# Optimization experiments

Hardware: AMD Instinct MI355X
Metric: run time of the kernel (lower is better)

The kernel has to match this reference:

```python
import jax, jax.numpy as jnp
import numpy as np

B, S, H, E, T, L = 128, 1024, 512, 512, 64, 128


def setup_inputs() -> dict:
    key = jax.random.key(0)
    ks = jax.random.split(key, 20)
    s = 0.02
    inp = {
        "sent_lengths": jax.random.randint(ks[0], (B,), 1, S, dtype=jnp.int32),
        "output_length": T,
        "decoder_input": jax.random.normal(ks[1], (B, E), jnp.float32),
        "h0": jax.random.normal(ks[2], (B, H), jnp.float32),
        "c0": jax.random.normal(ks[3], (B, H), jnp.float32),
        "context": jax.random.normal(ks[4], (B, S, H), jnp.float32),
        "cur_labels": jax.random.randint(ks[5], (B, T), 0, L, dtype=jnp.int32),
        "cur_max_nsymbs": jax.random.randint(ks[6], (B,), 0, 10, dtype=jnp.int32),
        # parameters
        "label_emb": jax.random.normal(ks[7], (L, E), jnp.float32) * s,
        "W_ih": jax.random.normal(ks[8], (4 * H, E), jnp.float32) * s,
        "b_ih": jnp.zeros((4 * H,), jnp.float32),
        "W_hh": jax.random.normal(ks[9], (4 * H, H), jnp.float32) * s,
        "b_hh": jnp.zeros((4 * H,), jnp.float32),
        "W_ho": jax.random.normal(ks[10], (H, 2 * H), jnp.float32) * s,
        "b_ho": jnp.zeros((H,), jnp.float32),
        "W_attn_in": jax.random.normal(ks[11], (H, H), jnp.float32) * s,
        "b_attn_in": jnp.zeros((H,), jnp.float32),
        "W_attn_ctx": jax.random.normal(ks[12], (H, H), jnp.float32) * s,
        "b_attn_ctx": jnp.zeros((H,), jnp.float32),
        "V": jax.random.uniform(ks[13], (H,), jnp.float32, -1.0, 1.0),
        "W_out": jax.random.normal(ks[14], (L, 2 * H + E), jnp.float32) * s,
        "b_out": jnp.zeros((L,), jnp.float32),
    }
    # padding_idx row of the label embedding is zero (torch nn.Embedding semantics)
    inp["label_emb"] = inp["label_emb"].at[0].set(0.0)
    return inp


def _decode(output_length, decoder_input, h0, c0, context, cur_labels,
            label_emb, W_ih, b_ih, W_hh, b_hh, W_ho, b_ho,
            W_attn_in, b_attn_in, W_attn_ctx, b_attn_ctx, V, W_out, b_out):
    # Precompute the 1x1-conv context projection once (identical math to per-step conv).
    ctx = jnp.einsum("bsh,gh->bsg", context, W_attn_ctx) + b_attn_ctx  # [B,S,H]

    # Teacher-forced input sequence: x_0 = decoder_input, x_i = emb(labels[:, i-1]).
    emb = label_emb[cur_labels]                     # [B,T,E]
    xs = jnp.concatenate(
        [decoder_input[None], jnp.swapaxes(emb, 0, 1)[: output_length - 1]], axis=0
    )                                               # [T,B,E]

    def step(carry, x):
        h, c = carry
        gates = x @ W_ih.T + b_ih + h @ W_hh.T + b_hh          # [B,4H]
        i_g, f_g, g_g, o_g = jnp.split(gates, 4, axis=1)
        c_t = jax.nn.sigmoid(f_g) * c + jax.nn.sigmoid(i_g) * jnp.tanh(g_g)
        h_lstm = jax.nn.sigmoid(o_g) * jnp.tanh(c_t)            # [B,H]
        # pointer attention
        inp = h_lstm @ W_attn_in.T + b_attn_in                  # [B,H]
        att = jnp.einsum("bsh,h->bs", jnp.tanh(inp[:, None, :] + ctx), V)
        alpha = jax.nn.softmax(att, axis=-1)                    # [B,S]
        weighted = jnp.einsum("bs,bsh->bh", alpha, ctx)         # [B,H]
        hidden_t = jnp.tanh(jnp.concatenate([weighted, h_lstm], 1) @ W_ho.T + b_ho)
        out = jnp.concatenate([hidden_t, weighted, x], 1) @ W_out.T + b_out  # [B,L]
        return (hidden_t, c_t), out

    (h_f, c_f), outs = jax.lax.scan(step, (h0, c0), xs)  # outs [T,B,L]
    outputs = jnp.transpose(outs, (1, 0, 2))             # [B,T,L]
    preds = jnp.argmax(outputs, axis=-1)                 # [B,T]
    return outputs, preds, h_f, c_f


def reference(sent_lengths, output_length, decoder_input, h0, c0, context,
              cur_labels, cur_max_nsymbs, label_emb, W_ih, b_ih, W_hh, b_hh,
              W_ho, b_ho, W_attn_in, b_attn_in, W_attn_ctx, b_attn_ctx, V,
              W_out, b_out):
    # cur_batch_len = len(sent_lengths) == B, so hidden slicing is a no-op here.
    # cur_max_nsymbs unused (constrained_decoding=None path).
    return _decode(output_length, decoder_input, h0, c0, context, cur_labels,
                   label_emb, W_ih, b_ih, W_hh, b_hh, W_ho, b_ho,
                   W_attn_in, b_attn_in, W_attn_ctx, b_attn_ctx, V, W_out, b_out)
```

## Files before the change

kernel.cpp:

```cpp
#include <hip/hip_runtime.h>
#include <hip/hip_bf16.h>
#include <math.h>

#define B_ 128
#define S_ 1024
#define H_ 512
#define E_ 512
#define T_ 64
#define L_ 128
#define G4H 2048
#define QS 8

typedef __attribute__((ext_vector_type(8))) short bf16x8;
typedef __attribute__((ext_vector_type(4))) float f32x4;

__device__ inline float sigmoidf_(float x) { return 1.f / (1.f + expf(-x)); }
__device__ inline float fast_tanhf_(float x) {
    float e = __expf(2.f * x);
    return 1.f - 2.f / (e + 1.f);
}
__device__ inline unsigned f2bf1(float f) {
    unsigned u = __float_as_uint(f);
    return (u + 0x7fffu + ((u >> 16) & 1u)) >> 16;
}

#define LDP 40
__global__ __launch_bounds__(256) void gemm_split(
    const float* __restrict__ A, int lda,
    const float* __restrict__ W, int ldw,
    const float* __restrict__ bias,
    const float* __restrict__ Cinit, int ldci,
    float* __restrict__ C, int ldc,
    int K, int act, int perm)
{
    __shared__ unsigned short Ah[128 * LDP];
    __shared__ unsigned short Al[128 * LDP];
    __shared__ unsigned short Bh[128 * LDP];
    __shared__ unsigned short Bl[128 * LDP];
    const int n0 = blockIdx.x * 128;
    const int m0 = blockIdx.y * 128;
    const int t = threadIdx.x;
    const int lane = t & 63, wv = t >> 6;
    const int wr = wv >> 1, wc = wv & 1;
    const int row = t >> 1, koff = (t & 1) * 16;

    f32x4 acc[4][4] = {};

    float av[16], wvv[16];
    {
        const float* ap = A + (size_t)(m0 + row) * lda + koff;
        const float* wp = W + (size_t)(n0 + row) * ldw + koff;
#pragma unroll
        for (int q = 0; q < 4; ++q) {
            *reinterpret_cast<float4*>(&av[q * 4]) = *reinterpret_cast<const float4*>(ap + q * 4);
            *reinterpret_cast<float4*>(&wvv[q * 4]) = *reinterpret_cast<const float4*>(wp + q * 4);
        }
// ... 62 lines not shown
            const float bs = bias ? bias[n] : 0.f;
#pragma unroll
            for (int r = 0; r < 4; ++r) {
                const int m = m0 + wr * 64 + i * 16 + (lane >> 4) * 4 + r;
                float v = acc[i][j][r] + bs;
                if (Cinit) v += Cinit[(size_t)m * ldci + n];
                if (act == 1) v = tanhf(v);
                size_t crow;
                if (perm) { int bb = m & 127, tt = m >> 7; crow = ((size_t)bb * T_ + tt) * ldc; }
                else crow = (size_t)m * ldc;
                C[crow + n] = v;
            }
        }
}

__global__ __launch_bounds__(128) void k_perm(
    const float* __restrict__ W_ih, const float* __restrict__ W_hh,
    const float* __restrict__ b_ih, const float* __restrict__ b_hh,
    float* __restrict__ Wip, float* __restrict__ Whp, float* __restrict__ bp)
{
    int rp = blockIdx.x;
    int h = rp >> 2, g = rp & 3;
    int src = g * 512 + h;
    int t = threadIdx.x;
    const float4* si = reinterpret_cast<const float4*>(W_ih + (size_t)src * 512);
    const float4* sh = reinterpret_cast<const float4*>(W_hh + (size_t)src * 512);
    float4* di = reinterpret_cast<float4*>(Wip + (size_t)rp * 512);
    float4* dh = reinterpret_cast<float4*>(Whp + (size_t)rp * 512);
    di[t] = si[t];
    dh[t] = sh[t];
    if (t == 0) bp[rp] = b_ih[src] + b_hh[src];
}

__global__ __launch_bounds__(256) void k_gateslstm(
    const float* __restrict__ hbuf,
    const float* __restrict__ Whp,
    const float* __restrict__ xproj_t,
    float* __restrict__ cbuf,
    float* __restrict__ hlstm)
{
    __shared__ float As[16][32];
    __shared__ float Ws[16][64];
    const int n0 = blockIdx.x * 64;
    const int m0 = blockIdx.y * 32;
    const int t = threadIdx.x;
    const int tx = t & 15;
    const int ty = t >> 4;
    const int alr = t >> 3, alk = (t & 7) * 2;
    const int wlr = t >> 2, wlk = (t & 3) * 4;

    float acc[2][4] = {};

    float2 pa = *reinterpret_cast<const float2*>(hbuf + (size_t)(m0 + alr) * 512 + alk);
    float4 pv = *reinterpret_cast<const float4*>(Whp + (size_t)(n0 + wlr) * 512 + wlk);

    for (int k0 = 0; k0 < 512; k0 += 16) {
        __syncthreads();
        As[alk + 0][alr] = pa.x; As[alk + 1][alr] = pa.y;
        Ws[wlk + 0][wlr] = pv.x; Ws[wlk + 1][wlr] = pv.y;
        Ws[wlk + 2][wlr] = pv.z; Ws[wlk + 3][wlr] = pv.w;
        __syncthreads();
        if (k0 + 16 < 512) {
            pa = *reinterpret_cast<const float2*>(hbuf + (size_t)(m0 + alr) * 512 + k0 + 16 + alk);
            pv = *reinterpret_cast<const float4*>(Whp + (size_t)(n0 + wlr) * 512 + k0 + 16 + wlk);
        }
#pragma unroll
        for (int kk = 0; kk < 16; ++kk) {
            float a[2], b[4];
            a[0] = As[kk][ty * 2]; a[1] = As[kk][ty * 2 + 1];
#pragma unroll
            for (int j = 0; j < 4; ++j) b[j] = Ws[kk][tx * 4 + j];
#pragma unroll
            for (int i = 0; i < 2; ++i)
#pragma unroll
                for (int j = 0; j < 4; ++j) acc[i][j] = fmaf(a[i], b[j], acc[i][j]);
        }
    }

    const int h = (n0 >> 2) + tx;
#pragma unroll
    for (int i = 0; i < 2; ++i) {
        const int b = m0 + ty * 2 + i;
        float4 xp = *reinterpret_cast<const float4*>(xproj_t + (size_t)b * G4H + n0 + tx * 4);
        float ig = sigmoidf_(acc[i][0] + xp.x);
        float fg = sigmoidf_(acc[i][1] + xp.y);
        float gg = tanhf(acc[i][2] + xp.z);
        float og = sigmoidf_(acc[i][3] + xp.w);
        float c = fg * cbuf[(size_t)b * 512 + h] + ig * gg;
        cbuf[(size_t)b * 512 + h] = c;
        hlstm[(size_t)b * 512 + h] = og * tanhf(c);
    }
}

__global__ __launch_bounds__(256) void gemm_stepk(
    const float* __restrict__ A, int lda,
    const float* __restrict__ W, int ldw,
    float* __restrict__ P, int N, int Kc)
{
    __shared__ float As[16][128];
    __shared__ float Ws[16][64];
    const int n0 = blockIdx.x * 64;
    const int k0 = blockIdx.y * Kc;
    const int t = threadIdx.x;
    const int tx = t & 15;
    const int ty = t >> 4;
    const int ar = t >> 1, akq = (t & 1) * 8;
    const int wr = t >> 2, wkq = (t & 3) * 4;

    float acc[8][4] = {};

    float4 a0 = *reinterpret_cast<const float4*>(A + (size_t)ar * lda + k0 + akq);
    float4 a1 = *reinterpret_cast<const float4*>(A + (size_t)ar * lda + k0 + akq + 4);
    float4 w0 = *reinterpret_cast<const float4*>(W + (size_t)(n0 + wr) * ldw + k0 + wkq);

    for (int kb = 0; kb < Kc; kb += 16) {
        __syncthreads();
        As[akq + 0][ar] = a0.x; As[akq + 1][ar] = a0.y; As[akq + 2][ar] = a0.z; As[akq + 3][ar] = a0.w;
        As[akq + 4][ar] = a1.x; As[akq + 5][ar] = a1.y; As[akq + 6][ar] = a1.z; As[akq + 7][ar] = a1.w;
        Ws[wkq + 0][wr] = w0.x; Ws[wkq + 1][wr] = w0.y; Ws[wkq + 2][wr] = w0.z; Ws[wkq + 3][wr] = w0.w;
        __syncthreads();
        if (kb + 16 < Kc) {
            a0 = *reinterpret_cast<const float4*>(A + (size_t)ar * lda + k0 + kb + 16 + akq);
            a1 = *reinterpret_cast<const float4*>(A + (size_t)ar * lda + k0 + kb + 16 + akq + 4);
            w0 = *reinterpret_cast<const float4*>(W + (size_t)(n0 + wr) * ldw + k0 + kb + 16 + wkq);
        }
#pragma unroll
        for (int kk = 0; kk < 16; ++kk) {
            float a[8], b[4];
#pragma unroll
            for (int i = 0; i < 8; ++i) a[i] = As[kk][ty * 8 + i];
#pragma unroll
            for (int j = 0; j < 4; ++j) b[j] = Ws[kk][tx * 4 + j];
#pragma unroll
            for (int i = 0; i < 8; ++i)
#pragma unroll
                for (int j = 0; j < 4; ++j) acc[i][j] = fmaf(a[i], b[j], acc[i][j]);
        }
    }

#pragma unroll
    for (int i = 0; i < 8; ++i) {
        const int m = ty * 8 + i;
#pragma unroll
        for (int j = 0; j < 4; ++j)
            P[((size_t)blockIdx.y * 128 + m) * N + n0 + tx * 4 + j] = acc[i][j];
    }
}

__global__ __launch_bounds__(256) void k_who(
    const float* __restrict__ pm, const float* __restrict__ pl,
    const float* __restrict__ pw, const float* __restrict__ hlstm,
    const float* __restrict__ W_ho,
    float* __restrict__ P, float* __restrict__ hist_t)
{
    __shared__ float As[16][128];
    __shared__ float Ws[16][64];
    __shared__ float eql[128][QS];
    const int n0 = blockIdx.x * 64;
    const int k0 = blockIdx.y * 128;
    const int t = threadIdx.x;
    const int tx = t & 15;
    const int ty = t >> 4;
    const int ar = t >> 1, akq = (t & 1) * 8;
    const int wr = t >> 2, wkq = (t & 3) * 4;
    const bool merge_side = (k0 < 512);
    const bool writer = (blockIdx.x == 0) && merge_side;

    if (merge_side && t < 128) {
        float mq[QS], eq[QS];
        float M = -INFINITY;
#pragma unroll
        for (int q = 0; q < QS; ++q) { mq[q] = pm[QS * t + q]; M = fmaxf(M, mq[q]); }
        float Lt = 0.f;
#pragma unroll
        for (int q = 0; q < QS; ++q) { eq[q] = __expf(mq[q] - M); Lt += eq[q] * pl[QS * t + q]; }
        float inv = 1.f / Lt;
#pragma unroll
        for (int q = 0; q < QS; ++q) eql[t][q] = eq[q] * inv;
    }
    __syncthreads();

    float acc[8][4] = {};
    float av[8];
    float4 w0;

    auto load_stage = [&](int kb) {
        const int kg = k0 + kb + akq;
        if (merge_side) {
#pragma unroll
            for (int e = 0; e < 8; ++e) av[e] = 0.f;
#pragma unroll
            for (int q = 0; q < QS; ++q) {
                const float* pr = pw + (size_t)(QS * ar + q) * 512 + kg;
                float4 pa = *reinterpret_cast<const float4*>(pr);
                float4 pb = *reinterpret_cast<const float4*>(pr + 4);
                float qw = eql[ar][q];
                av[0] = fmaf(qw, pa.x, av[0]); av[1] = fmaf(qw, pa.y, av[1]);
                av[2] = fmaf(qw, pa.z, av[2]); av[3] = fmaf(qw, pa.w, av[3]);
                av[4] = fmaf(qw, pb.x, av[4]); av[5] = fmaf(qw, pb.y, av[5]);
                av[6] = fmaf(qw, pb.z, av[6]); av[7] = fmaf(qw, pb.w, av[7]);
            }
            if (writer) {
                *reinterpret_cast<float4*>(hist_t + (size_t)ar * 1024 + 512 + kg) = *reinterpret_cast<float4*>(&av[0]);
                *reinterpret_cast<float4*>(hist_t + (size_t)ar * 1024 + 512 + kg + 4) = *reinterpret_cast<float4*>(&av[4]);
            }
        } else {
            *reinterpret_cast<float4*>(&av[0]) = *reinterpret_cast<const float4*>(hlstm + (size_t)ar * 512 + kg - 512);
            *reinterpret_cast<float4*>(&av[4]) = *reinterpret_cast<const float4*>(hlstm + (size_t)ar * 512 + kg - 512 + 4);
        }
        w0 = *reinterpret_cast<const float4*>(W_ho + (size_t)(n0 + wr) * 1024 + k0 + kb + wkq);
    };

    load_stage(0);

    for (int kb = 0; kb < 128; kb += 16) {
        __syncthreads();
        As[akq + 0][ar] = av[0]; As[akq + 1][ar] = av[1]; As[akq + 2][ar] = av[2]; As[akq + 3][ar] = av[3];
        As[akq + 4][ar] = av[4]; As[akq + 5][ar] = av[5]; As[akq + 6][ar] = av[6]; As[akq + 7][ar] = av[7];
        Ws[wkq + 0][wr] = w0.x; Ws[wkq + 1][wr] = w0.y; Ws[wkq + 2][wr] = w0.z; Ws[wkq + 3][wr] = w0.w;
        __syncthreads();
        if (kb + 16 < 128) load_stage(kb + 16);
#pragma unroll
        for (int kk = 0; kk < 16; ++kk) {
            float a[8], b[4];
#pragma unroll
            for (int i = 0; i < 8; ++i) a[i] = As[kk][ty * 8 + i];
#pragma unroll
            for (int j = 0; j < 4; ++j) b[j] = Ws[kk][tx * 4 + j];
#pragma unroll
            for (int i = 0; i < 8; ++i)
#pragma unroll
                for (int j = 0; j < 4; ++j) acc[i][j] = fmaf(a[i], b[j], acc[i][j]);
        }
    }

#pragma unroll
    for (int i = 0; i < 8; ++i) {
        const int m = ty * 8 + i;
#pragma unroll
        for (int j = 0; j < 4; ++j)
            P[((size_t)blockIdx.y * 128 + m) * 512 + n0 + tx * 4 + j] = acc[i][j];
    }
}

__global__ void k_embed(const float* __restrict__ dec_in, const int* __restrict__ labels,
                        const float* __restrict__ emb, float* __restrict__ X)
{
    size_t total = (size_t)T_ * B_ * E_;
    for (size_t i = (size_t)blockIdx.x * blockDim.x + threadIdx.x; i < total;
         i += (size_t)gridDim.x * blockDim.x) {
        int e = (int)(i % E_);
        int b = (int)((i / E_) % B_);
        int t = (int)(i / ((size_t)E_ * B_));
        float v;
        if (t == 0) v = dec_in[b * E_ + e];
        else {
            int lab = labels[b * T_ + (t - 1)];
            v = emb[(size_t)lab * E_ + e];
        }
        X[i] = v;
    }
}

__global__ void k_init(const float* __restrict__ h0, const float* __restrict__ c0,
                       float* __restrict__ hbuf, float* __restrict__ cbuf)
{
    int i = blockIdx.x * blockDim.x + threadIdx.x;
    hbuf[i] = h0[i];
    cbuf[i] = c0[i];
}

__global__ __launch_bounds__(512) void k_attn(const float* __restrict__ ctx,
    const float* __restrict__ Pa, const float* __restrict__ b_ain,
    const float* __restrict__ Vv,
    float* __restrict__ pm, float* __restrict__ pl, float* __restrict__ pw)
{
    int blk = blockIdx.x;
    int b = blk >> 3, q = blk & 7;
    int tid = threadIdx.x, lane = tid & 63, wv = tid >> 6;

    __shared__ float inp_sh[512];
    inp_sh[tid] = Pa[(size_t)b * 512 + tid]
                + Pa[(size_t)(128 + b) * 512 + tid]
                + Pa[(size_t)(256 + b) * 512 + tid]
                + Pa[(size_t)(384 + b) * 512 + tid]
                + b_ain[tid];
    __syncthreads();

    float inpr[8], vr[8];
    {
        const float4* v4 = reinterpret_cast<const float4*>(Vv) + lane * 2;
        *(float4*)&vr[0] = v4[0];   *(float4*)&vr[4] = v4[1];
#pragma unroll
        for (int k = 0; k < 8; ++k) inpr[k] = inp_sh[lane * 8 + k];
    }
    const float* sp = ctx + ((size_t)b * S_ + q * 128 + wv * 16) * H_ + lane * 8;

    float m = -INFINITY, l = 0.f, w[8] = {};
    float4 c0 = *reinterpret_cast<const float4*>(sp);
    float4 c1 = *reinterpret_cast<const float4*>(sp + 4);
    for (int si = 0; si < 16; ++si) {
        float4 u0 = c0, u1 = c1;
        if (si < 15) {
            c0 = *reinterpret_cast<const float4*>(sp + (size_t)(si + 1) * H_);
            c1 = *reinterpret_cast<const float4*>(sp + (size_t)(si + 1) * H_ + 4);
        }
        float c8[8];
        *(float4*)&c8[0] = u0; *(float4*)&c8[4] = u1;
        float t = 0.f;
#pragma unroll
        for (int k = 0; k < 8; ++k) t = fmaf(fast_tanhf_(inpr[k] + c8[k]), vr[k], t);
#pragma unroll
        for (int off = 32; off > 0; off >>= 1) t += __shfl_xor(t, off);
        float mn = fmaxf(m, t);
        float sc = __expf(m - mn);
        float p  = __expf(t - mn);
        l = l * sc + p;
#pragma unroll
        for (int k = 0; k < 8; ++k) w[k] = w[k] * sc + p * c8[k];
        m = mn;
    }

    __shared__ float wl[8 * 512];
    __shared__ float ml[8], ll[8];
#pragma unroll
    for (int k = 0; k < 8; ++k) wl[wv * 512 + lane * 8 + k] = w[k];
    if (lane == 0) { ml[wv] = m; ll[wv] = l; }
    __syncthreads();

    float M = ml[0];
#pragma unroll
    for (int u = 1; u < 8; ++u) M = fmaxf(M, ml[u]);
    float lt = 0.f, wt = 0.f;
#pragma unroll
    for (int u = 0; u < 8; ++u) {
        float e = __expf(ml[u] - M);
        lt += e * ll[u];
        wt += e * wl[u * 512 + tid];
    }
    if (tid == 0) { pm[blk] = M; pl[blk] = lt; }
    pw[(size_t)blk * 512 + tid] = wt;
}

__global__ __launch_bounds__(256) void k_whofin(const float* __restrict__ Po,
    const float* __restrict__ b_ho, float* __restrict__ hbuf, float* __restrict__ hist_t)
{
    int i = blockIdx.x * blockDim.x + threadIdx.x;
    int b = i >> 9, h = i & 511;
    float v = b_ho[h];
#pragma unroll
    for (int ks = 0; ks < 8; ++ks) v += Po[((size_t)ks * 128 + b) * 512 + h];
    v = tanhf(v);
    hbuf[i] = v;
    hist_t[(size_t)b * 1024 + h] = v;
}

__global__ __launch_bounds__(128) void k_argmax(const float* __restrict__ outp,
                                                float* __restrict__ preds)
{
    int row = blockIdx.x;
    int tid = threadIdx.x;
    float v = outp[(size_t)row * L_ + tid];
    int idx = tid;
#pragma unroll
    for (int off = 32; off > 0; off >>= 1) {
        float ov = __shfl_xor(v, off);
        int oi = __shfl_xor(idx, off);
        if (ov > v || (ov == v && oi < idx)) { v = ov; idx = oi; }
    }
    __shared__ float sv[2];
    __shared__ int si[2];
    if ((tid & 63) == 0) { sv[tid >> 6] = v; si[tid >> 6] = idx; }
    __syncthreads();
    if (tid == 0) {
        float v0 = sv[0], v1 = sv[1];
        int i0 = si[0], i1 = si[1];
        int r = (v1 > v0 || (v1 == v0 && i1 < i0)) ? i1 : i0;
        preds[row] = (float)r;
    }
}

__global__ void k_final(const float* __restrict__ hbuf, const float* __restrict__ cbuf,
                        float* __restrict__ hf, float* __restrict__ cf)
{
    int i = blockIdx.x * blockDim.x + threadIdx.x;
    hf[i] = hbuf[i];
    cf[i] = cbuf[i];
}

extern "C" void kernel_launch(void* const* d_in, const int* in_sizes, int n_in,
                              void* d_out, int out_size, void* d_ws, size_t ws_size,
                              hipStream_t stream)
{
    const float* dec_in  = (const float*)d_in[2];
    const float* h0      = (const float*)d_in[3];
    const float* c0      = (const float*)d_in[4];
    const float* context = (const float*)d_in[5];
    const int*   labels  = (const int*)d_in[6];
    const float* emb     = (const float*)d_in[8];
    const float* W_ih    = (const float*)d_in[9];
    const float* b_ih    = (const float*)d_in[10];
    const float* W_hh    = (const float*)d_in[11];
    const float* b_hh    = (const float*)d_in[12];
    const float* W_ho    = (const float*)d_in[13];
    const float* b_ho    = (const float*)d_in[14];
    const float* W_ain   = (const float*)d_in[15];
    const float* b_ain   = (const float*)d_in[16];
    const float* W_actx  = (const float*)d_in[17];
    const float* b_actx  = (const float*)d_in[18];
    const float* Vv      = (const float*)d_in[19];
    const float* W_out   = (const float*)d_in[20];
    const float* b_out   = (const float*)d_in[21];

    float* ws = (float*)d_ws;
    float* X     = ws; ws += (size_t)T_ * B_ * E_;
    float* xproj = ws; ws += (size_t)T_ * B_ * G4H;
    float* xout  = ws; ws += (size_t)T_ * B_ * L_;
    float* ctx   = ws; ws += (size_t)B_ * S_ * H_;
    float* hist  = ws; ws += (size_t)T_ * B_ * 1024;
    float* Wip   = ws; ws += (size_t)G4H * 512;
    float* Whp   = ws; ws += (size_t)G4H * 512;
    float* bp    = ws; ws += G4H;
    float* Pa    = ws; ws += (size_t)4 * B_ * H_;
    float* Po    = ws; ws += (size_t)8 * B_ * H_;
    float* cbuf  = ws; ws += (size_t)B_ * H_;
    float* hbuf  = ws; ws += (size_t)B_ * H_;
    float* hlstm = ws; ws += (size_t)B_ * H_;
    float* pm    = ws; ws += (size_t)B_ * QS;
    float* pl    = ws; ws += (size_t)B_ * QS;
    float* pw    = ws; ws += (size_t)B_ * QS * 512;

    float* out_logits = (float*)d_out;
    float* out_preds  = out_logits + (size_t)B_ * T_ * L_;
    float* out_hf     = out_preds + (size_t)B_ * T_;
    float* out_cf     = out_hf + (size_t)B_ * H_;

    k_embed<<<2048, 256, 0, stream>>>(dec_in, labels, emb, X);
    k_init<<<256, 256, 0, stream>>>(h0, c0, hbuf, cbuf);
    k_perm<<<G4H, 128, 0, stream>>>(W_ih, W_hh, b_ih, b_hh, Wip, Whp, bp);
    gemm_split<<<dim3(16, 64), 256, 0, stream>>>(X, E_, Wip, E_, bp, nullptr, 0,
                                                 xproj, G4H, E_, 0, 0);
    gemm_split<<<dim3(1, 64), 256, 0, stream>>>(X, E_, W_out + 1024, 1536, b_out, nullptr, 0,
                                                xout, L_, E_, 0, 0);
    gemm_split<<<dim3(4, 1024), 256, 0, stream>>>(context, H_, W_actx, H_, b_actx, nullptr, 0,
                                                  ctx, H_, H_, 0, 0);

    for (int t = 0; t < T_; ++t) {
        float* hist_t = hist + (size_t)t * B_ * 1024;
        k_gateslstm<<<dim3(32, 4), 256, 0, stream>>>(hbuf, Whp,
                                                     xproj + (size_t)t * B_ * G4H,
                                                     cbuf, hlstm);
        gemm_stepk<<<dim3(8, 4), 256, 0, stream>>>(hlstm, H_, W_ain, H_, Pa, H_, 128);
        k_attn<<<B_ * QS, 512, 0, stream>>>(ctx, Pa, b_ain, Vv, pm, pl, pw);
        k_who<<<dim3(8, 8), 256, 0, stream>>>(pm, pl, pw, hlstm, W_ho, Po, hist_t);
        k_whofin<<<256, 256, 0, stream>>>(Po, b_ho, hbuf, hist_t);
    }

    gemm_split<<<dim3(1, 64), 256, 0, stream>>>(hist, 1024, W_out, 1536, nullptr,
                                                xout, L_, out_logits, L_, 1024, 0, 1);
    k_argmax<<<B_ * T_, 128, 0, stream>>>(out_logits, out_preds);
    k_final<<<256, 256, 0, stream>>>(hbuf, cbuf, out_hf, out_cf);
}
```

Baseline: 7.470 ms.

## Fuse hidden-state finalization into LSTM gate kernel and split attention projection further

Removes the per-step k_whofin launch. The next step's k_gateslstm now reduces the W_ho split-K partials, applies tanh on the fly while loading its A operand, and has block column 0 write the history row for the previous step. The last step's finalization moves into a single k_fin63 kernel that also writes the final h/c outputs, which replaces k_final. The attention-input projection GEMM is also split into 8 K-slices instead of 4 to launch more blocks, and k_attn sums the 8 partials. In exchange, every gate block redundantly recomputes the 8-way reduction and tanh for its A tiles, which adds global reads and transcendental work inside the recurrent loop.

After: 8.467 ms. +13.4%, slower.

```diff
diff --git a/kernel.cpp b/kernel.cpp
--- a/kernel.cpp
+++ b/kernel.cpp
@@ -152,10 +152,14 @@
 
 __global__ __launch_bounds__(256) void k_gateslstm(
     const float* __restrict__ hbuf,
+    const float* __restrict__ Po,
+    const float* __restrict__ b_ho,
     const float* __restrict__ Whp,
     const float* __restrict__ xproj_t,
     float* __restrict__ cbuf,
-    float* __restrict__ hlstm)
+    float* __restrict__ hlstm,
+    float* __restrict__ hist_prev,
+    int fused)
 {
     __shared__ float As[16][32];
     __shared__ float Ws[16][64];
@@ -169,7 +173,22 @@
 
     float acc[2][4] = {};
 
-    float2 pa = *reinterpret_cast<const float2*>(hbuf + (size_t)(m0 + alr) * 512 + alk);
+    auto load_pa = [&](int k0) -> float2 {
+        const int row = m0 + alr, k = k0 + alk;
+        if (!fused) return *reinterpret_cast<const float2*>(hbuf + (size_t)row * 512 + k);
+        float s0 = b_ho[k], s1 = b_ho[k + 1];
+#pragma unroll
+        for (int ks = 0; ks < 8; ++ks) {
+            float2 p = *reinterpret_cast<const float2*>(Po + ((size_t)ks * 128 + row) * 512 + k);
+            s0 += p.x; s1 += p.y;
+        }
+        float2 r; r.x = tanhf(s0); r.y = tanhf(s1);
+        if (blockIdx.x == 0)
+            *reinterpret_cast<float2*>(hist_prev + (size_t)row * 1024 + k) = r;
+        return r;
+    };
+
+    float2 pa = load_pa(0);
     float4 pv = *reinterpret_cast<const float4*>(Whp + (size_t)(n0 + wlr) * 512 + wlk);
 
     for (int k0 = 0; k0 < 512; k0 += 16) {
@@ -179,7 +198,7 @@
         Ws[wlk + 2][wlr] = pv.z; Ws[wlk + 3][wlr] = pv.w;
         __syncthreads();
         if (k0 + 16 < 512) {
-            pa = *reinterpret_cast<const float2*>(hbuf + (size_t)(m0 + alr) * 512 + k0 + 16 + alk);
+            pa = load_pa(k0 + 16);
             pv = *reinterpret_cast<const float4*>(Whp + (size_t)(n0 + wlr) * 512 + k0 + 16 + wlk);
         }
 #pragma unroll
@@ -398,11 +417,12 @@
     int tid = threadIdx.x, lane = tid & 63, wv = tid >> 6;
 
     __shared__ float inp_sh[512];
-    inp_sh[tid] = Pa[(size_t)b * 512 + tid]
-                + Pa[(size_t)(128 + b) * 512 + tid]
-                + Pa[(size_t)(256 + b) * 512 + tid]
-                + Pa[(size_t)(384 + b) * 512 + tid]
-                + b_ain[tid];
+    {
+        float s = b_ain[tid];
+#pragma unroll
+        for (int ks = 0; ks < 8; ++ks) s += Pa[((size_t)ks * 128 + b) * 512 + tid];
+        inp_sh[tid] = s;
+    }
     __syncthreads();
 
     float inpr[8], vr[8];
@@ -415,6 +435,24 @@
     const float* sp = ctx + ((size_t)b * S_ + q * 128 + wv * 16) * H_ + lane * 8;
 
     float m = -INFINITY, l = 0.f, w[8] = {};
+
+    auto process = [&](float4 u0, float4 u1) {
+        float c8[8];
+        *(float4*)&c8[0] = u0; *(float4*)&c8[4] = u1;
+        float t = 0.f;
+#pragma unroll
+        for (int k = 0; k < 8; ++k) t = fmaf(fast_tanhf_(inpr[k] + c8[k]), vr[k], t);
+#pragma unroll
+        for (int off = 32; off > 0; off >>= 1) t += __shfl_xor(t, off);
+        float mn = fmaxf(m, t);
+        float sc = __expf(m - mn);
+        float p  = __expf(t - mn);
+        l = l * sc + p;
+#pragma unroll
+        for (int k = 0; k < 8; ++k) w[k] = w[k] * sc + p * c8[k];
+        m = mn;
+    };
+
     float4 c0 = *reinterpret_cast<const float4*>(sp);
     float4 c1 = *reinterpret_cast<const float4*>(sp + 4);
     for (int si = 0; si < 16; ++si) {
@@ -423,20 +461,7 @@
             c0 = *reinterpret_cast<const float4*>(sp + (size_t)(si + 1) * H_);
             c1 = *reinterpret_cast<const float4*>(sp + (size_t)(si + 1) * H_ + 4);
         }
-        float c8[8];
-        *(float4*)&c8[0] = u0; *(float4*)&c8[4] = u1;
-        float t = 0.f;
-#pragma unroll
-        for (int k = 0; k < 8; ++k) t = fmaf(fast_tanhf_(inpr[k] + c8[k]), vr[k], t);
-#pragma unroll
-        for (int off = 32; off > 0; off >>= 1) t += __shfl_xor(t, off);
-        float mn = fmaxf(m, t);
-        float sc = __expf(m - mn);
-        float p  = __expf(t - mn);
-        l = l * sc + p;
-#pragma unroll
-        for (int k = 0; k < 8; ++k) w[k] = w[k] * sc + p * c8[k];
-        m = mn;
+        process(u0, u1);
     }
 
     __shared__ float wl[8 * 512];
@@ -460,8 +485,9 @@
     pw[(size_t)blk * 512 + tid] = wt;
 }
 
-__global__ __launch_bounds__(256) void k_whofin(const float* __restrict__ Po,
-    const float* __restrict__ b_ho, float* __restrict__ hbuf, float* __restrict__ hist_t)
+__global__ __launch_bounds__(256) void k_fin63(const float* __restrict__ Po,
+    const float* __restrict__ b_ho, const float* __restrict__ cbuf,
+    float* __restrict__ hist63, float* __restrict__ hf, float* __restrict__ cf)
 {
     int i = blockIdx.x * blockDim.x + threadIdx.x;
     int b = i >> 9, h = i & 511;
@@ -469,8 +495,9 @@
 #pragma unroll
     for (int ks = 0; ks < 8; ++ks) v += Po[((size_t)ks * 128 + b) * 512 + h];
     v = tanhf(v);
-    hbuf[i] = v;
-    hist_t[(size_t)b * 1024 + h] = v;
+    hf[i] = v;
+    cf[i] = cbuf[i];
+    hist63[(size_t)b * 1024 + h] = v;
 }
 
 __global__ __launch_bounds__(128) void k_argmax(const float* __restrict__ outp,
@@ -496,14 +523,6 @@
         int r = (v1 > v0 || (v1 == v0 && i1 < i0)) ? i1 : i0;
         preds[row] = (float)r;
     }
-}
-
-__global__ void k_final(const float* __restrict__ hbuf, const float* __restrict__ cbuf,
-                        float* __restrict__ hf, float* __restrict__ cf)
-{
-    int i = blockIdx.x * blockDim.x + threadIdx.x;
-    hf[i] = hbuf[i];
-    cf[i] = cbuf[i];
 }
 
 extern "C" void kernel_launch(void* const* d_in, const int* in_sizes, int n_in,
@@ -539,7 +558,7 @@
     float* Wip   = ws; ws += (size_t)G4H * 512;
     float* Whp   = ws; ws += (size_t)G4H * 512;
     float* bp    = ws; ws += G4H;
-    float* Pa    = ws; ws += (size_t)4 * B_ * H_;
+    float* Pa    = ws; ws += (size_t)8 * B_ * H_;
     float* Po    = ws; ws += (size_t)8 * B_ * H_;
     float* cbuf  = ws; ws += (size_t)B_ * H_;
     float* hbuf  = ws; ws += (size_t)B_ * H_;
@@ -565,17 +584,18 @@
 
     for (int t = 0; t < T_; ++t) {
         float* hist_t = hist + (size_t)t * B_ * 1024;
-        k_gateslstm<<<dim3(32, 4), 256, 0, stream>>>(hbuf, Whp,
+        float* hist_prev = hist + (size_t)(t > 0 ? t - 1 : 0) * B_ * 1024;
+        k_gateslstm<<<dim3(32, 4), 256, 0, stream>>>(hbuf, Po, b_ho, Whp,
                                                      xproj + (size_t)t * B_ * G4H,
-                                                     cbuf, hlstm);
-        gemm_stepk<<<dim3(8, 4), 256, 0, stream>>>(hlstm, H_, W_ain, H_, Pa, H_, 128);
+                                                     cbuf, hlstm, hist_prev, t > 0 ? 1 : 0);
+        gemm_stepk<<<dim3(8, 8), 256, 0, stream>>>(hlstm, H_, W_ain, H_, Pa, H_, 64);
         k_attn<<<B_ * QS, 512, 0, stream>>>(ctx, Pa, b_ain, Vv, pm, pl, pw);
         k_who<<<dim3(8, 8), 256, 0, stream>>>(pm, pl, pw, hlstm, W_ho, Po, hist_t);
-        k_whofin<<<256, 256, 0, stream>>>(Po, b_ho, hbuf, hist_t);
-    }
-
+    }
+
+    k_fin63<<<256, 256, 0, stream>>>(Po, b_ho, cbuf,
+                                     hist + (size_t)63 * B_ * 1024, out_hf, out_cf);
     gemm_split<<<dim3(1, 64), 256, 0, stream>>>(hist, 1024, W_out, 1536, nullptr,
                                                 xout, L_, out_logits, L_, 1024, 0, 1);
     k_argmax<<<B_ * T_, 128, 0, stream>>>(out_logits, out_preds);
-    k_final<<<256, 256, 0, stream>>>(hbuf, cbuf, out_hf, out_cf);
-}
+}
```

## Fuse per-step decoder kernels into one persistent kernel with grid barriers

Applied to the files above, without the earlier changes.

Replaces the five launches per timestep (LSTM gates, attention-input projection, attention, W_ho GEMM, finalize) with a single persistent 256-block kernel that loops over all 64 steps and separates phases with an atomic-counter grid barrier. It also repartitions the work: 2 attention splits per batch row instead of 8, the W_ho GEMM done in full K inside 32 blocks (no separate reduction kernel), and the final h/c written directly. The aim is to remove about 320 kernel launches and their gaps. In exchange, all 256 blocks must be co-resident for the spin barrier to work, and some phases now run on only a few blocks.

Result: slower. 13.86 ms (+85.6%).

```diff
diff --git a/kernel.cpp b/kernel.cpp
--- a/kernel.cpp
+++ b/kernel.cpp
@@ -9,7 +9,8 @@
 #define T_ 64
 #define L_ 128
 #define G4H 2048
-#define QS 8
+#define NB 256
+#define NT 512
 
 typedef __attribute__((ext_vector_type(8))) short bf16x8;
 typedef __attribute__((ext_vector_type(4))) float f32x4;
@@ -22,6 +23,21 @@
 __device__ inline unsigned f2bf1(float f) {
     unsigned u = __float_as_uint(f);
     return (u + 0x7fffu + ((u >> 16) & 1u)) >> 16;
+}
+
+__device__ inline void gbar(unsigned* cnt, unsigned target) {
+    __syncthreads();
+    if (threadIdx.x == 0) {
+        __threadfence();
+        __hip_atomic_fetch_add(cnt, 1u, __ATOMIC_RELAXED, __HIP_MEMORY_SCOPE_AGENT);
+        unsigned it = 0;
+        while (__hip_atomic_load(cnt, __ATOMIC_RELAXED, __HIP_MEMORY_SCOPE_AGENT) < target) {
+            __builtin_amdgcn_s_sleep(2);
+            if (++it > (1u << 26)) break;
+        }
+        __threadfence();
+    }
+    __syncthreads();
 }
 
 #define LDP 40
@@ -150,217 +166,6 @@
     if (t == 0) bp[rp] = b_ih[src] + b_hh[src];
 }
 
-__global__ __launch_bounds__(256) void k_gateslstm(
-    const float* __restrict__ hbuf,
-    const float* __restrict__ Whp,
-    const float* __restrict__ xproj_t,
-    float* __restrict__ cbuf,
-    float* __restrict__ hlstm)
-{
-    __shared__ float As[16][32];
-    __shared__ float Ws[16][64];
-    const int n0 = blockIdx.x * 64;
-    const int m0 = blockIdx.y * 32;
-    const int t = threadIdx.x;
-    const int tx = t & 15;
-    const int ty = t >> 4;
-    const int alr = t >> 3, alk = (t & 7) * 2;
-    const int wlr = t >> 2, wlk = (t & 3) * 4;
-
-    float acc[2][4] = {};
-
-    float2 pa = *reinterpret_cast<const float2*>(hbuf + (size_t)(m0 + alr) * 512 + alk);
-    float4 pv = *reinterpret_cast<const float4*>(Whp + (size_t)(n0 + wlr) * 512 + wlk);
-
-    for (int k0 = 0; k0 < 512; k0 += 16) {
-        __syncthreads();
-        As[alk + 0][alr] = pa.x; As[alk + 1][alr] = pa.y;
-        Ws[wlk + 0][wlr] = pv.x; Ws[wlk + 1][wlr] = pv.y;
-        Ws[wlk + 2][wlr] = pv.z; Ws[wlk + 3][wlr] = pv.w;
-        __syncthreads();
-        if (k0 + 16 < 512) {
-            pa = *reinterpret_cast<const float2*>(hbuf + (size_t)(m0 + alr) * 512 + k0 + 16 + alk);
-            pv = *reinterpret_cast<const float4*>(Whp + (size_t)(n0 + wlr) * 512 + k0 + 16 + wlk);
-        }
-#pragma unroll
-        for (int kk = 0; kk < 16; ++kk) {
-            float a[2], b[4];
-            a[0] = As[kk][ty * 2]; a[1] = As[kk][ty * 2 + 1];
-#pragma unroll
-            for (int j = 0; j < 4; ++j) b[j] = Ws[kk][tx * 4 + j];
-#pragma unroll
-            for (int i = 0; i < 2; ++i)
-#pragma unroll
-                for (int j = 0; j < 4; ++j) acc[i][j] = fmaf(a[i], b[j], acc[i][j]);
-        }
-    }
-
-    const int h = (n0 >> 2) + tx;
-#pragma unroll
-    for (int i = 0; i < 2; ++i) {
-        const int b = m0 + ty * 2 + i;
-        float4 xp = *reinterpret_cast<const float4*>(xproj_t + (size_t)b * G4H + n0 + tx * 4);
-        float ig = sigmoidf_(acc[i][0] + xp.x);
-        float fg = sigmoidf_(acc[i][1] + xp.y);
-        float gg = tanhf(acc[i][2] + xp.z);
-        float og = sigmoidf_(acc[i][3] + xp.w);
-        float c = fg * cbuf[(size_t)b * 512 + h] + ig * gg;
-        cbuf[(size_t)b * 512 + h] = c;
-        hlstm[(size_t)b * 512 + h] = og * tanhf(c);
-    }
-}
-
-__global__ __launch_bounds__(256) void gemm_stepk(
-    const float* __restrict__ A, int lda,
-    const float* __restrict__ W, int ldw,
-    float* __restrict__ P, int N, int Kc)
-{
-    __shared__ float As[16][128];
-    __shared__ float Ws[16][64];
-    const int n0 = blockIdx.x * 64;
-    const int k0 = blockIdx.y * Kc;
-    const int t = threadIdx.x;
-    const int tx = t & 15;
-    const int ty = t >> 4;
-    const int ar = t >> 1, akq = (t & 1) * 8;
-    const int wr = t >> 2, wkq = (t & 3) * 4;
-
-    float acc[8][4] = {};
-
-    float4 a0 = *reinterpret_cast<const float4*>(A + (size_t)ar * lda + k0 + akq);
-    float4 a1 = *reinterpret_cast<const float4*>(A + (size_t)ar * lda + k0 + akq + 4);
-    float4 w0 = *reinterpret_cast<const float4*>(W + (size_t)(n0 + wr) * ldw + k0 + wkq);
-
-    for (int kb = 0; kb < Kc; kb += 16) {
-        __syncthreads();
-        As[akq + 0][ar] = a0.x; As[akq + 1][ar] = a0.y; As[akq + 2][ar] = a0.z; As[akq + 3][ar] = a0.w;
-        As[akq + 4][ar] = a1.x; As[akq + 5][ar] = a1.y; As[akq + 6][ar] = a1.z; As[akq + 7][ar] = a1.w;
-        Ws[wkq + 0][wr] = w0.x; Ws[wkq + 1][wr] = w0.y; Ws[wkq + 2][wr] = w0.z; Ws[wkq + 3][wr] = w0.w;
-        __syncthreads();
-        if (kb + 16 < Kc) {
-            a0 = *reinterpret_cast<const float4*>(A + (size_t)ar * lda + k0 + kb + 16 + akq);
-            a1 = *reinterpret_cast<const float4*>(A + (size_t)ar * lda + k0 + kb + 16 + akq + 4);
-            w0 = *reinterpret_cast<const float4*>(W + (size_t)(n0 + wr) * ldw + k0 + kb + 16 + wkq);
-        }
-#pragma unroll
-        for (int kk = 0; kk < 16; ++kk) {
-            float a[8], b[4];
-#pragma unroll
-            for (int i = 0; i < 8; ++i) a[i] = As[kk][ty * 8 + i];
-#pragma unroll
-            for (int j = 0; j < 4; ++j) b[j] = Ws[kk][tx * 4 + j];
-#pragma unroll
-            for (int i = 0; i < 8; ++i)
-#pragma unroll
-                for (int j = 0; j < 4; ++j) acc[i][j] = fmaf(a[i], b[j], acc[i][j]);
-        }
-    }
-
-#pragma unroll
-    for (int i = 0; i < 8; ++i) {
-        const int m = ty * 8 + i;
-#pragma unroll
-        for (int j = 0; j < 4; ++j)
-            P[((size_t)blockIdx.y * 128 + m) * N + n0 + tx * 4 + j] = acc[i][j];
-    }
-}
-
-__global__ __launch_bounds__(256) void k_who(
-    const float* __restrict__ pm, const float* __restrict__ pl,
-    const float* __restrict__ pw, const float* __restrict__ hlstm,
-    const float* __restrict__ W_ho,
-    float* __restrict__ P, float* __restrict__ hist_t)
-{
-    __shared__ float As[16][128];
-    __shared__ float Ws[16][64];
-    __shared__ float eql[128][QS];
-    const int n0 = blockIdx.x * 64;
-    const int k0 = blockIdx.y * 128;
-    const int t = threadIdx.x;
-    const int tx = t & 15;
-    const int ty = t >> 4;
-    const int ar = t >> 1, akq = (t & 1) * 8;
-    const int wr = t >> 2, wkq = (t & 3) * 4;
-    const bool merge_side = (k0 < 512);
-    const bool writer = (blockIdx.x == 0) && merge_side;
-
-    if (merge_side && t < 128) {
-        float mq[QS], eq[QS];
-        float M = -INFINITY;
-#pragma unroll
-        for (int q = 0; q < QS; ++q) { mq[q] = pm[QS * t + q]; M = fmaxf(M, mq[q]); }
-        float Lt = 0.f;
-#pragma unroll
-        for (int q = 0; q < QS; ++q) { eq[q] = __expf(mq[q] - M); Lt += eq[q] * pl[QS * t + q]; }
-        float inv = 1.f / Lt;
-#pragma unroll
-        for (int q = 0; q < QS; ++q) eql[t][q] = eq[q] * inv;
-    }
-    __syncthreads();
-
-    float acc[8][4] = {};
-    float av[8];
-    float4 w0;
-
-    auto load_stage = [&](int kb) {
-        const int kg = k0 + kb + akq;
-        if (merge_side) {
-#pragma unroll
-            for (int e = 0; e < 8; ++e) av[e] = 0.f;
-#pragma unroll
-            for (int q = 0; q < QS; ++q) {
-                const float* pr = pw + (size_t)(QS * ar + q) * 512 + kg;
-                float4 pa = *reinterpret_cast<const float4*>(pr);
-                float4 pb = *reinterpret_cast<const float4*>(pr + 4);
-                float qw = eql[ar][q];
-                av[0] = fmaf(qw, pa.x, av[0]); av[1] = fmaf(qw, pa.y, av[1]);
-                av[2] = fmaf(qw, pa.z, av[2]); av[3] = fmaf(qw, pa.w, av[3]);
-                av[4] = fmaf(qw, pb.x, av[4]); av[5] = fmaf(qw, pb.y, av[5]);
-                av[6] = fmaf(qw, pb.z, av[6]); av[7] = fmaf(qw, pb.w, av[7]);
-            }
-            if (writer) {
-                *reinterpret_cast<float4*>(hist_t + (size_t)ar * 1024 + 512 + kg) = *reinterpret_cast<float4*>(&av[0]);
-                *reinterpret_cast<float4*>(hist_t + (size_t)ar * 1024 + 512 + kg + 4) = *reinterpret_cast<float4*>(&av[4]);
-            }
-        } else {
-            *reinterpret_cast<float4*>(&av[0]) = *reinterpret_cast<const float4*>(hlstm + (size_t)ar * 512 + kg - 512);
-            *reinterpret_cast<float4*>(&av[4]) = *reinterpret_cast<const float4*>(hlstm + (size_t)ar * 512 + kg - 512 + 4);
-        }
-        w0 = *reinterpret_cast<const float4*>(W_ho + (size_t)(n0 + wr) * 1024 + k0 + kb + wkq);
-    };
-
-    load_stage(0);
-
-    for (int kb = 0; kb < 128; kb += 16) {
-        __syncthreads();
-        As[akq + 0][ar] = av[0]; As[akq + 1][ar] = av[1]; As[akq + 2][ar] = av[2]; As[akq + 3][ar] = av[3];
-        As[akq + 4][ar] = av[4]; As[akq + 5][ar] = av[5]; As[akq + 6][ar] = av[6]; As[akq + 7][ar] = av[7];
-        Ws[wkq + 0][wr] = w0.x; Ws[wkq + 1][wr] = w0.y; Ws[wkq + 2][wr] = w0.z; Ws[wkq + 3][wr] = w0.w;
-        __syncthreads();
-        if (kb + 16 < 128) load_stage(kb + 16);
-#pragma unroll
-        for (int kk = 0; kk < 16; ++kk) {
-            float a[8], b[4];
-#pragma unroll
-            for (int i = 0; i < 8; ++i) a[i] = As[kk][ty * 8 + i];
-#pragma unroll
-            for (int j = 0; j < 4; ++j) b[j] = Ws[kk][tx * 4 + j];
-#pragma unroll
-            for (int i = 0; i < 8; ++i)
-#pragma unroll
-                for (int j = 0; j < 4; ++j) acc[i][j] = fmaf(a[i], b[j], acc[i][j]);
-        }
-    }
-
-#pragma unroll
-    for (int i = 0; i < 8; ++i) {
-        const int m = ty * 8 + i;
-#pragma unroll
-        for (int j = 0; j < 4; ++j)
-            P[((size_t)blockIdx.y * 128 + m) * 512 + n0 + tx * 4 + j] = acc[i][j];
-    }
-}
-
 __global__ void k_embed(const float* __restrict__ dec_in, const int* __restrict__ labels,
                         const float* __restrict__ emb, float* __restrict__ X)
 {
@@ -381,96 +186,236 @@
 }
 
 __global__ void k_init(const float* __restrict__ h0, const float* __restrict__ c0,
-                       float* __restrict__ hbuf, float* __restrict__ cbuf)
+                       float* __restrict__ hbuf, float* __restrict__ cbuf,
+                       unsigned* __restrict__ cnt)
 {
     int i = blockIdx.x * blockDim.x + threadIdx.x;
     hbuf[i] = h0[i];
     cbuf[i] = c0[i];
-}
-
-__global__ __launch_bounds__(512) void k_attn(const float* __restrict__ ctx,
-    const float* __restrict__ Pa, const float* __restrict__ b_ain,
-    const float* __restrict__ Vv,
-    float* __restrict__ pm, float* __restrict__ pl, float* __restrict__ pw)
-{
-    int blk = blockIdx.x;
-    int b = blk >> 3, q = blk & 7;
-    int tid = threadIdx.x, lane = tid & 63, wv = tid >> 6;
-
-    __shared__ float inp_sh[512];
-    inp_sh[tid] = Pa[(size_t)b * 512 + tid]
-                + Pa[(size_t)(128 + b) * 512 + tid]
-                + Pa[(size_t)(256 + b) * 512 + tid]
-                + Pa[(size_t)(384 + b) * 512 + tid]
-                + b_ain[tid];
-    __syncthreads();
-
-    float inpr[8], vr[8];
-    {
-        const float4* v4 = reinterpret_cast<const float4*>(Vv) + lane * 2;
-        *(float4*)&vr[0] = v4[0];   *(float4*)&vr[4] = v4[1];
-#pragma unroll
-        for (int k = 0; k < 8; ++k) inpr[k] = inp_sh[lane * 8 + k];
-    }
-    const float* sp = ctx + ((size_t)b * S_ + q * 128 + wv * 16) * H_ + lane * 8;
-
-    float m = -INFINITY, l = 0.f, w[8] = {};
-    float4 c0 = *reinterpret_cast<const float4*>(sp);
-    float4 c1 = *reinterpret_cast<const float4*>(sp + 4);
-    for (int si = 0; si < 16; ++si) {
-        float4 u0 = c0, u1 = c1;
-        if (si < 15) {
-            c0 = *reinterpret_cast<const float4*>(sp + (size_t)(si + 1) * H_);
-            c1 = *reinterpret_cast<const float4*>(sp + (size_t)(si + 1) * H_ + 4);
-        }
-        float c8[8];
-        *(float4*)&c8[0] = u0; *(float4*)&c8[4] = u1;
-        float t = 0.f;
-#pragma unroll
-        for (int k = 0; k < 8; ++k) t = fmaf(fast_tanhf_(inpr[k] + c8[k]), vr[k], t);
-#pragma unroll
-        for (int off = 32; off > 0; off >>= 1) t += __shfl_xor(t, off);
-        float mn = fmaxf(m, t);
-        float sc = __expf(m - mn);
-        float p  = __expf(t - mn);
-        l = l * sc + p;
-#pragma unroll
-        for (int k = 0; k < 8; ++k) w[k] = w[k] * sc + p * c8[k];
-        m = mn;
-    }
-
-    __shared__ float wl[8 * 512];
-    __shared__ float ml[8], ll[8];
-#pragma unroll
-    for (int k = 0; k < 8; ++k) wl[wv * 512 + lane * 8 + k] = w[k];
-    if (lane == 0) { ml[wv] = m; ll[wv] = l; }
-    __syncthreads();
-
-    float M = ml[0];
-#pragma unroll
-    for (int u = 1; u < 8; ++u) M = fmaxf(M, ml[u]);
-    float lt = 0.f, wt = 0.f;
-#pragma unroll
-    for (int u = 0; u < 8; ++u) {
-        float e = __expf(ml[u] - M);
-        lt += e * ll[u];
-        wt += e * wl[u * 512 + tid];
-    }
-    if (tid == 0) { pm[blk] = M; pl[blk] = lt; }
-    pw[(size_t)blk * 512 + tid] = wt;
-}
-
-__global__ __launch_bounds__(256) void k_whofin(const float* __restrict__ Po,
-    const float* __restrict__ b_ho, float* __restrict__ hbuf, float* __restrict__ hist_t)
-{
-    int i = blockIdx.x * blockDim.x + threadIdx.x;
-    int b = i >> 9, h = i & 511;
-    float v = b_ho[h];
-#pragma unroll
-    for (int ks = 0; ks < 8; ++ks) v += Po[((size_t)ks * 128 + b) * 512 + h];
-    v = tanhf(v);
-    hbuf[i] = v;
-    hist_t[(size_t)b * 1024 + h] = v;
+    if (i == 0) cnt[0] = 0u;
+}
+
+__global__ __launch_bounds__(NT, 2) void k_loop(
+    const float* __restrict__ Whp, const float* __restrict__ xproj,
+    const float* __restrict__ W_ain, const float* __restrict__ b_ain,
+    const float* __restrict__ Vv, const float* __restrict__ W_ho,
+    const float* __restrict__ b_ho, const float* __restrict__ ctx,
+    float* __restrict__ cbuf, float* __restrict__ hbuf, float* __restrict__ hlstm,
+    float* __restrict__ Pa, float* __restrict__ pm, float* __restrict__ pl,
+    float* __restrict__ pw, float* __restrict__ hist,
+    float* __restrict__ out_hf, float* __restrict__ out_cf,
+    unsigned* __restrict__ cnt)
+{
+    const int bid = blockIdx.x;
+    const int t0 = threadIdx.x;
+
+    __shared__ float shbuf[4624];
+    float (*As)[32] = reinterpret_cast<float(*)[32]>(shbuf);
+    float (*Ws)[64] = reinterpret_cast<float(*)[64]>(shbuf + 512);
+    float (*eql)[2] = reinterpret_cast<float(*)[2]>(shbuf + 1536);
+    float* inp = shbuf;
+    float* wl  = shbuf + 512;
+    float* ml  = shbuf + 4608;
+    float* ll  = shbuf + 4616;
+
+    const int ty = t0 >> 4;
+    const int tx = t0 & 15;
+    const int alr = t0 & 31, alk = t0 >> 5;
+    const int wlr = t0 & 63, wk2 = (t0 >> 6) * 2;
+    const int lane = t0 & 63, wv = t0 >> 6;
+
+    unsigned ep = 0;
+
+    for (int t = 0; t < T_; ++t) {
+        if (bid < 128) {
+            const int m0 = (bid >> 5) * 32;
+            const int n0 = (bid & 31) * 64;
+            float acc[4] = {};
+            float pa = hbuf[(size_t)(m0 + alr) * 512 + alk];
+            float2 pv = *reinterpret_cast<const float2*>(Whp + (size_t)(n0 + wlr) * 512 + wk2);
+            for (int k0 = 0; k0 < 512; k0 += 16) {
+                __syncthreads();
+                As[alk][alr] = pa;
+                Ws[wk2][wlr] = pv.x; Ws[wk2 + 1][wlr] = pv.y;
+                __syncthreads();
+                if (k0 + 16 < 512) {
+                    pa = hbuf[(size_t)(m0 + alr) * 512 + k0 + 16 + alk];
+                    pv = *reinterpret_cast<const float2*>(Whp + (size_t)(n0 + wlr) * 512 + k0 + 16 + wk2);
+                }
+#pragma unroll
+                for (int kk = 0; kk < 16; ++kk) {
+                    float a = As[kk][ty];
+#pragma unroll
+                    for (int j = 0; j < 4; ++j) acc[j] = fmaf(a, Ws[kk][tx * 4 + j], acc[j]);
+                }
+            }
+            const int h = (n0 >> 2) + tx;
+            const int b = m0 + ty;
+            float4 xp = *reinterpret_cast<const float4*>(xproj + (size_t)t * B_ * G4H + (size_t)b * G4H + n0 + tx * 4);
+            float ig = sigmoidf_(acc[0] + xp.x);
+            float fg = sigmoidf_(acc[1] + xp.y);
+            float gg = tanhf(acc[2] + xp.z);
+            float og = sigmoidf_(acc[3] + xp.w);
+            float c = fg * cbuf[(size_t)b * 512 + h] + ig * gg;
+            cbuf[(size_t)b * 512 + h] = c;
+            hlstm[(size_t)b * 512 + h] = og * tanhf(c);
+            if (t == T_ - 1) out_cf[(size_t)b * 512 + h] = c;
+        }
+        gbar(cnt, ++ep * NB);
+
+        {
+            const int ks = bid >> 5;
+            const int m0 = ((bid & 31) >> 3) * 32;
+            const int n0 = (bid & 7) * 64;
+            const int kb = ks * 64;
+            float acc[4] = {};
+            float pa = hlstm[(size_t)(m0 + alr) * 512 + kb + alk];
+            float2 pv = *reinterpret_cast<const float2*>(W_ain + (size_t)(n0 + wlr) * 512 + kb + wk2);
+            for (int k0 = 0; k0 < 64; k0 += 16) {
+                __syncthreads();
+                As[alk][alr] = pa;
+                Ws[wk2][wlr] = pv.x; Ws[wk2 + 1][wlr] = pv.y;
+                __syncthreads();
+                if (k0 + 16 < 64) {
+                    pa = hlstm[(size_t)(m0 + alr) * 512 + kb + k0 + 16 + alk];
+                    pv = *reinterpret_cast<const float2*>(W_ain + (size_t)(n0 + wlr) * 512 + kb + k0 + 16 + wk2);
+                }
+#pragma unroll
+                for (int kk = 0; kk < 16; ++kk) {
+                    float a = As[kk][ty];
+#pragma unroll
+                    for (int j = 0; j < 4; ++j) acc[j] = fmaf(a, Ws[kk][tx * 4 + j], acc[j]);
+                }
+            }
+#pragma unroll
+            for (int j = 0; j < 4; ++j)
+                Pa[((size_t)ks * 128 + m0 + ty) * 512 + n0 + tx * 4 + j] = acc[j];
+        }
+        gbar(cnt, ++ep * NB);
+
+        {
+            const int b = bid >> 1, half = bid & 1;
+            float s = b_ain[t0];
+#pragma unroll
+            for (int ks = 0; ks < 8; ++ks) s += Pa[((size_t)ks * 128 + b) * 512 + t0];
+            inp[t0] = s;
+            __syncthreads();
+            float inpr[8], vr[8];
+            {
+                const float4* v4 = reinterpret_cast<const float4*>(Vv) + lane * 2;
+                *(float4*)&vr[0] = v4[0]; *(float4*)&vr[4] = v4[1];
+#pragma unroll
+                for (int k = 0; k < 8; ++k) inpr[k] = inp[lane * 8 + k];
+            }
+            const float* sp = ctx + ((size_t)b * S_ + half * 512 + wv * 64) * 512 + lane * 8;
+
+            float m = -INFINITY, l = 0.f, w[8] = {};
+            float4 p0[4], p1[4];
+#pragma unroll
+            for (int j = 0; j < 4; ++j) {
+                p0[j] = *reinterpret_cast<const float4*>(sp + (size_t)j * 512);
+                p1[j] = *reinterpret_cast<const float4*>(sp + (size_t)j * 512 + 4);
+            }
+            for (int so = 0; so < 64; so += 4) {
+                const bool pf = (so + 4 < 64);
+#pragma unroll
+                for (int j = 0; j < 4; ++j) {
+                    float c8[8];
+                    *(float4*)&c8[0] = p0[j]; *(float4*)&c8[4] = p1[j];
+                    if (pf) {
+                        p0[j] = *reinterpret_cast<const float4*>(sp + (size_t)(so + 4 + j) * 512);
+                        p1[j] = *reinterpret_cast<const float4*>(sp + (size_t)(so + 4 + j) * 512 + 4);
+                    }
+                    float tt = 0.f;
+#pragma unroll
+                    for (int k = 0; k < 8; ++k) tt = fmaf(fast_tanhf_(inpr[k] + c8[k]), vr[k], tt);
+#pragma unroll
+                    for (int off = 32; off > 0; off >>= 1) tt += __shfl_xor(tt, off);
+                    float mn = fmaxf(m, tt);
+                    float sc = __expf(m - mn);
+                    float p  = __expf(tt - mn);
+                    l = l * sc + p;
+#pragma unroll
+                    for (int k = 0; k < 8; ++k) w[k] = w[k] * sc + p * c8[k];
+                    m = mn;
+                }
+            }
+#pragma unroll
+            for (int k = 0; k < 8; ++k) wl[wv * 512 + lane * 8 + k] = w[k];
+            if (lane == 0) { ml[wv] = m; ll[wv] = l; }
+            __syncthreads();
+            float M = ml[0];
+#pragma unroll
+            for (int u = 1; u < 8; ++u) M = fmaxf(M, ml[u]);
+            float lt = 0.f, wt = 0.f;
+#pragma unroll
+            for (int u = 0; u < 8; ++u) {
+                float e = __expf(ml[u] - M);
+                lt += e * ll[u];
+                wt += e * wl[u * 512 + t0];
+            }
+            if (t0 == 0) { pm[bid] = M; pl[bid] = lt; }
+            pw[(size_t)bid * 512 + t0] = wt;
+        }
+        gbar(cnt, ++ep * NB);
+
+        if (bid < 32) {
+            const int m0 = (bid >> 3) * 32;
+            const int nt = bid & 7;
+            const int n0 = nt * 64;
+            if (t0 < 32) {
+                const int row = m0 + t0;
+                float q0 = pm[row * 2], q1 = pm[row * 2 + 1];
+                float M = fmaxf(q0, q1);
+                float e0 = __expf(q0 - M), e1 = __expf(q1 - M);
+                float Lt = e0 * pl[row * 2] + e1 * pl[row * 2 + 1];
+                float inv = 1.f / Lt;
+                eql[t0][0] = e0 * inv; eql[t0][1] = e1 * inv;
+            }
+            __syncthreads();
+            float* hist_t = hist + (size_t)t * B_ * 1024;
+            float acc[4] = {};
+            auto ld_a = [&](int k0) -> float {
+                const int row = m0 + alr;
+                const int k = k0 + alk;
+                if (k0 < 512) {
+                    float v = eql[alr][0] * pw[((size_t)row * 2) * 512 + k]
+                            + eql[alr][1] * pw[((size_t)row * 2 + 1) * 512 + k];
+                    if (nt == 0) hist_t[(size_t)row * 1024 + 512 + k] = v;
+                    return v;
+                }
+                return hlstm[(size_t)row * 512 + k - 512];
+            };
+            float pa = ld_a(0);
+            float2 pv = *reinterpret_cast<const float2*>(W_ho + (size_t)(n0 + wlr) * 1024 + wk2);
+            for (int k0 = 0; k0 < 1024; k0 += 16) {
+                __syncthreads();
+                As[alk][alr] = pa;
+                Ws[wk2][wlr] = pv.x; Ws[wk2 + 1][wlr] = pv.y;
+                __syncthreads();
+                if (k0 + 16 < 1024) {
+                    pa = ld_a(k0 + 16);
+                    pv = *reinterpret_cast<const float2*>(W_ho + (size_t)(n0 + wlr) * 1024 + k0 + 16 + wk2);
+                }
+#pragma unroll
+                for (int kk = 0; kk < 16; ++kk) {
+                    float a = As[kk][ty];
+#pragma unroll
+                    for (int j = 0; j < 4; ++j) acc[j] = fmaf(a, Ws[kk][tx * 4 + j], acc[j]);
+                }
+            }
+            const int b = m0 + ty;
+#pragma unroll
+            for (int j = 0; j < 4; ++j) {
+                const int n = n0 + tx * 4 + j;
+                float v = tanhf(acc[j] + b_ho[n]);
+                hbuf[(size_t)b * 512 + n] = v;
+                hist_t[(size_t)b * 1024 + n] = v;
+                if (t == T_ - 1) out_hf[(size_t)b * 512 + n] = v;
+            }
+        }
+        gbar(cnt, ++ep * NB);
+    }
 }
 
 __global__ __launch_bounds__(128) void k_argmax(const float* __restrict__ outp,
@@ -496,14 +441,6 @@
         int r = (v1 > v0 || (v1 == v0 && i1 < i0)) ? i1 : i0;
         preds[row] = (float)r;
     }
-}
-
-__global__ void k_final(const float* __restrict__ hbuf, const float* __restrict__ cbuf,
-                        float* __restrict__ hf, float* __restrict__ cf)
-{
-    int i = blockIdx.x * blockDim.x + threadIdx.x;
-    hf[i] = hbuf[i];
-    cf[i] = cbuf[i];
 }
 
 extern "C" void kernel_launch(void* const* d_in, const int* in_sizes, int n_in,
@@ -531,6 +468,7 @@
     const float* b_out   = (const float*)d_in[21];
 
     float* ws = (float*)d_ws;
+    unsigned* cnt = (unsigned*)ws; ws += 64;
     float* X     = ws; ws += (size_t)T_ * B_ * E_;
     float* xproj = ws; ws += (size_t)T_ * B_ * G4H;
     float* xout  = ws; ws += (size_t)T_ * B_ * L_;
@@ -539,14 +477,13 @@
     float* Wip   = ws; ws += (size_t)G4H * 512;
     float* Whp   = ws; ws += (size_t)G4H * 512;
     float* bp    = ws; ws += G4H;
-    float* Pa    = ws; ws += (size_t)4 * B_ * H_;
-    float* Po    = ws; ws += (size_t)8 * B_ * H_;
+    float* Pa    = ws; ws += (size_t)8 * B_ * H_;
     float* cbuf  = ws; ws += (size_t)B_ * H_;
     float* hbuf  = ws; ws += (size_t)B_ * H_;
     float* hlstm = ws; ws += (size_t)B_ * H_;
-    float* pm    = ws; ws += (size_t)B_ * QS;
-    float* pl    = ws; ws += (size_t)B_ * QS;
-    float* pw    = ws; ws += (size_t)B_ * QS * 512;
+    float* pm    = ws; ws += (size_t)B_ * 2;
+    float* pl    = ws; ws += (size_t)B_ * 2;
+    float* pw    = ws; ws += (size_t)B_ * 2 * 512;
 
     float* out_logits = (float*)d_out;
     float* out_preds  = out_logits + (size_t)B_ * T_ * L_;
@@ -554,7 +491,7 @@
     float* out_cf     = out_hf + (size_t)B_ * H_;
 
     k_embed<<<2048, 256, 0, stream>>>(dec_in, labels, emb, X);
-    k_init<<<256, 256, 0, stream>>>(h0, c0, hbuf, cbuf);
+    k_init<<<256, 256, 0, stream>>>(h0, c0, hbuf, cbuf, cnt);
     k_perm<<<G4H, 128, 0, stream>>>(W_ih, W_hh, b_ih, b_hh, Wip, Whp, bp);
     gemm_split<<<dim3(16, 64), 256, 0, stream>>>(X, E_, Wip, E_, bp, nullptr, 0,
                                                  xproj, G4H, E_, 0, 0);
@@ -563,19 +500,11 @@
     gemm_split<<<dim3(4, 1024), 256, 0, stream>>>(context, H_, W_actx, H_, b_actx, nullptr, 0,
                                                   ctx, H_, H_, 0, 0);
 
-    for (int t = 0; t < T_; ++t) {
-        float* hist_t = hist + (size_t)t * B_ * 1024;
-        k_gateslstm<<<dim3(32, 4), 256, 0, stream>>>(hbuf, Whp,
-                                                     xproj + (size_t)t * B_ * G4H,
-                                                     cbuf, hlstm);
-        gemm_stepk<<<dim3(8, 4), 256, 0, stream>>>(hlstm, H_, W_ain, H_, Pa, H_, 128);
-        k_attn<<<B_ * QS, 512, 0, stream>>>(ctx, Pa, b_ain, Vv, pm, pl, pw);
-        k_who<<<dim3(8, 8), 256, 0, stream>>>(pm, pl, pw, hlstm, W_ho, Po, hist_t);
-        k_whofin<<<256, 256, 0, stream>>>(Po, b_ho, hbuf, hist_t);
-    }
+    k_loop<<<NB, NT, 0, stream>>>(Whp, xproj, W_ain, b_ain, Vv, W_ho, b_ho, ctx,
+                                  cbuf, hbuf, hlstm, Pa, pm, pl, pw, hist,
+                                  out_hf, out_cf, cnt);
 
     gemm_split<<<dim3(1, 64), 256, 0, stream>>>(hist, 1024, W_out, 1536, nullptr,
                                                 xout, L_, out_logits, L_, 1024, 0, 1);
     k_argmax<<<B_ * T_, 128, 0, stream>>>(out_logits, out_preds);
-    k_final<<<256, 256, 0, stream>>>(hbuf, cbuf, out_hf, out_cf);
-}
+}
```
